# Kernel optimization log

Measured on AMD Instinct MI355X. Metric: run time of the kernel, lower is better.

The kernel has to match this reference:

```python
import jax, jax.numpy as jnp
import numpy as np

N_NODES = 200000
MAX_DEG = 128
S1, S2 = 25, 10  # neighbor sample sizes per hop (GraphSAGE defaults)


def setup_inputs() -> dict:
    key = jax.random.key(0)
    ks = jax.random.split(key, 9)
    F, H, C, B = 256, 128, 41, 1024
    return {
        "node_ids": jax.random.randint(ks[0], (B,), 0, N_NODES, dtype=jnp.int32),
        "features": jax.random.normal(ks[1], (N_NODES, F), dtype=jnp.float32),
        "adj_info": jax.random.randint(ks[2], (N_NODES, MAX_DEG), 0, N_NODES, dtype=jnp.int32),
        "W_self1": jax.random.normal(ks[3], (F, H), dtype=jnp.float32) * 0.05,
        "W_neigh1": jax.random.normal(ks[4], (F, H), dtype=jnp.float32) * 0.05,
        "W_self2": jax.random.normal(ks[5], (2 * H, H), dtype=jnp.float32) * 0.05,
        "W_neigh2": jax.random.normal(ks[6], (2 * H, H), dtype=jnp.float32) * 0.05,
        "W_pred": jax.random.normal(ks[7], (2 * H, C), dtype=jnp.float32) * 0.05,
        "b_pred": jnp.zeros((C,), dtype=jnp.float32),
    }


def _sample(adj_info, node_ids):
    """Uniform neighbor sampling: hop1 [B,S1], hop2 [B,S1,S2]."""
    k1, k2 = jax.random.split(jax.random.key(42))
    B = node_ids.shape[0]
    cols1 = jax.random.randint(k1, (B, S1), 0, MAX_DEG)
    hop1 = jnp.take_along_axis(adj_info[node_ids], cols1, axis=1)  # [B,S1]
    cols2 = jax.random.randint(k2, (B * S1, S2), 0, MAX_DEG)
    hop2 = jnp.take_along_axis(adj_info[hop1.reshape(-1)], cols2, axis=1)
    return hop1, hop2.reshape(B, S1, S2)


def _mean_agg(self_f, neigh_f, Ws, Wn, act):
    # GraphSAGE MeanAggregator with concat: [self@Ws ; mean(neigh)@Wn]
    neigh = neigh_f.mean(axis=-2)
    return act(jnp.concatenate([self_f @ Ws, neigh @ Wn], axis=-1))


def reference(node_ids, features, adj_info, W_self1, W_neigh1, W_self2, W_neigh2, W_pred, b_pred):
    hop1, hop2 = _sample(adj_info, node_ids)
    f0 = features[node_ids]      # [B,F]
    f1 = features[hop1]          # [B,S1,F]
    f2 = features[hop2]          # [B,S1,S2,F]

    h0 = _mean_agg(f0, f1, W_self1, W_neigh1, jax.nn.relu)   # [B,2H]
    h1 = _mean_agg(f1, f2, W_self1, W_neigh1, jax.nn.relu)   # [B,S1,2H]
    h = _mean_agg(h0, h1, W_self2, W_neigh2, lambda x: x)    # [B,2H]

    # tf.math.l2_normalize(x, 1): x * rsqrt(max(sum(x^2), 1e-12))
    h = h * jax.lax.rsqrt(jnp.maximum(jnp.sum(h * h, axis=1, keepdims=True), 1e-12))
    logits = h @ W_pred + b_pred
    return jax.nn.softmax(logits, axis=-1)
```

## Files before the change

### kernel.cpp

```cpp
#include <hip/hip_runtime.h>
#include <cstdint>
#include <cstddef>

#define BATCH 1024
#define S1 25
#define S2 10
#define FDIM 256
#define HDIM 128
#define NCLS 41
#define MAXDEG 128

typedef __attribute__((ext_vector_type(8))) short bf16x8;
typedef __attribute__((ext_vector_type(4))) float f32x4;

__host__ __device__ static inline void tf2x32(uint32_t k0, uint32_t k1,
                                              uint32_t c0, uint32_t c1,
                                              uint32_t& o0, uint32_t& o1) {
  const uint32_t ks2 = k0 ^ k1 ^ 0x1BD11BDAu;
  uint32_t x0 = c0 + k0, x1 = c1 + k1;
#define TFR(r) { x0 += x1; x1 = (x1 << (r)) | (x1 >> (32 - (r))); x1 ^= x0; }
  TFR(13) TFR(15) TFR(26) TFR(6)
  x0 += k1;  x1 += ks2 + 1u;
  TFR(17) TFR(29) TFR(16) TFR(24)
  x0 += ks2; x1 += k0 + 2u;
  TFR(13) TFR(15) TFR(26) TFR(6)
  x0 += k0;  x1 += k1 + 3u;
  TFR(17) TFR(29) TFR(16) TFR(24)
  x0 += k1;  x1 += ks2 + 4u;
  TFR(13) TFR(15) TFR(26) TFR(6)
  x0 += ks2; x1 += k0 + 5u;
#undef TFR
  o0 = x0; o1 = x1;
}

__device__ static inline uint32_t rand_bits_at(uint32_t kb0, uint32_t kb1, uint32_t j) {
  uint32_t o0, o1;
  tf2x32(kb0, kb1, 0u, j, o0, o1);
  return o0 ^ o1;
}

__device__ static inline ushort f2bf(float x) {
  uint32_t u = __float_as_uint(x);
  return (ushort)((u + 0x7fffu + ((u >> 16) & 1u)) >> 16);
}

__global__ __launch_bounds__(256)
void prep_kernel(const int* __restrict__ node_ids, const float* __restrict__ feat,
                 const int* __restrict__ adj,
                 const float* __restrict__ Ws1, const float* __restrict__ Wn1,
                 int* __restrict__ hop1g, ushort* __restrict__ n2m,
                 float* __restrict__ n1m, ushort* __restrict__ WbT,
                 float* __restrict__ h1m,
                 uint32_t kb1_0, uint32_t kb1_1, uint32_t kb2_0, uint32_t kb2_1) {
  const int blk = blockIdx.x;
  const int t = threadIdx.x;
  if (blk < 6400) {
    const int wave = t >> 6, lane = t & 63;
    const int g = blk * 4 + wave;
    const int b = g / S1;
    int hop1v = 0;
    if (lane == 0) {
      uint32_t c1 = rand_bits_at(kb1_0, kb1_1, (uint32_t)g) & (MAXDEG - 1);
      hop1v = adj[(size_t)node_ids[b] * MAXDEG + c1];
    }
    hop1v = __shfl(hop1v, 0, 64);
    if (lane == 0) hop1g[g] = hop1v;
    int r2id = 0;
    if (lane < S2) {
      uint32_t c2 = rand_bits_at(kb2_0, kb2_1, (uint32_t)(g * S2 + lane)) & (MAXDEG - 1);
      r2id = adj[(size_t)hop1v * MAXDEG + c2];
    }
    float4 acc = make_float4(0.f, 0.f, 0.f, 0.f);
#pragma unroll
    for (int r = 0; r < S2; ++r) {
      int rid = __shfl(r2id, r, 64);
      float4 v = ((const float4*)(feat + (size_t)rid * FDIM))[lane];
      acc.x += v.x; acc.y += v.y; acc.z += v.z; acc.w += v.w;
    }
    const float inv = 1.f / S2;
    ushort4 o;
    o.x = f2bf(acc.x * inv); o.y = f2bf(acc.y * inv);
    o.z = f2bf(acc.z * inv); o.w = f2bf(acc.w * inv);
    *(ushort4*)(n2m + (size_t)g * FDIM + lane * 4) = o;
  } else if (blk < 6656) {
    const int wave = t >> 6, lane = t & 63;
    const int b = (blk - 6400) * 4 + wave;
    int h1v = 0;
    if (lane < S1) {
      uint32_t c1 = rand_bits_at(kb1_0, kb1_1, (uint32_t)(b * S1 + lane)) & (MAXDEG - 1);
      h1v = adj[(size_t)node_ids[b] * MAXDEG + c1];
    }
    float4 acc = make_float4(0.f, 0.f, 0.f, 0.f);
#pragma unroll
    for (int r = 0; r < S1; ++r) {
      int rid = __shfl(h1v, r, 64);
      float4 v = ((const float4*)(feat + (size_t)rid * FDIM))[lane];
      acc.x += v.x; acc.y += v.y; acc.z += v.z; acc.w += v.w;
    }
    const float inv = 1.f / S1;
    acc.x *= inv; acc.y *= inv; acc.z *= inv; acc.w *= inv;
    ((float4*)(n1m + (size_t)b * FDIM))[lane] = acc;
  } else if (blk < 6912) {
    const int idx = blk - 6656;
    const int h = idx >> 7, n = idx & 127;
    const float* W = h ? Wn1 : Ws1;
    WbT[(size_t)idx * FDIM + t] = f2bf(W[(size_t)t * HDIM + n]);
  } else {
    const int i = (blk - 6912) * 256 + t;
    ((float4*)h1m)[i] = make_float4(0.f, 0.f, 0.f, 0.f);
  }
}

__global__ __launch_bounds__(256, 2)
void mfma_h1_kernel(const int* __restrict__ hop1g, const float* __restrict__ feat,
                    const ushort* __restrict__ n2m, const ushort* __restrict__ WbT,
                    float* __restrict__ h1m) {
  const int half = blockIdx.y;
  const ushort* Bmat = WbT + (size_t)half * HDIM * FDIM;
  const int m0 = blockIdx.x * 64;
  const int tid = threadIdx.x;
  const int wave = tid >> 6;
  const int lane = tid & 63;
  const int lq = lane >> 4;
  const int lr = lane & 15;

  __shared__ ushort As[64][40];
  __shared__ ushort Bs[128][40];
  __shared__ float  Cs[64][132];
  __shared__ int rowid[64];

  if (half == 0 && tid < 64) rowid[tid] = hop1g[m0 + tid];
  __syncthreads();

  f32x4 acc[4][2];
#pragma unroll
  for (int rt = 0; rt < 4; ++rt)
#pragma unroll
    for (int ct = 0; ct < 2; ++ct) acc[rt][ct] = (f32x4)(0.f);

  for (int k0 = 0; k0 < FDIM; k0 += 32) {
    const int row = tid >> 2, kc = (tid & 3) * 8;
    if (half == 0) {
      const float* rp = feat + (size_t)rowid[row] * FDIM + k0 + kc;
      float4 v0 = *(const float4*)rp;
      float4 v1 = *(const float4*)(rp + 4);
      union { ushort u[8]; int4 v; } pk;
      pk.u[0] = f2bf(v0.x); pk.u[1] = f2bf(v0.y); pk.u[2] = f2bf(v0.z); pk.u[3] = f2bf(v0.w);
      pk.u[4] = f2bf(v1.x); pk.u[5] = f2bf(v1.y); pk.u[6] = f2bf(v1.z); pk.u[7] = f2bf(v1.w);
      *(int4*)&As[row][kc] = pk.v;
    } else {
      int4 v = *(const int4*)(n2m + (size_t)(m0 + row) * FDIM + k0 + kc);
      *(int4*)&As[row][kc] = v;
    }
#pragma unroll
    for (int i = 0; i < 2; ++i) {
      int idx = tid + i * 256;
      int n = idx >> 2, kc2 = (idx & 3) * 8;
      int4 v = *(const int4*)(Bmat + (size_t)n * FDIM + k0 + kc2);
      *(int4*)&Bs[n][kc2] = v;
    }
    __syncthreads();

    bf16x8 af[4];
#pragma unroll
    for (int rt = 0; rt < 4; ++rt)
      af[rt] = *(const bf16x8*)&As[rt * 16 + lr][lq * 8];
#pragma unroll
    for (int ct = 0; ct < 2; ++ct) {
      bf16x8 bf = *(const bf16x8*)&Bs[wave * 32 + ct * 16 + lr][lq * 8];
#pragma unroll
      for (int rt = 0; rt < 4; ++rt)
        acc[rt][ct] = __builtin_amdgcn_mfma_f32_16x16x32_bf16(af[rt], bf, acc[rt][ct], 0, 0, 0);
    }
    __syncthreads();
  }

#pragma unroll
  for (int rt = 0; rt < 4; ++rt)
#pragma unroll
    for (int ct = 0; ct < 2; ++ct)
#pragma unroll
      for (int r = 0; r < 4; ++r)
        Cs[rt * 16 + lq * 4 + r][wave * 32 + ct * 16 + lr] = fmaxf(acc[rt][ct][r], 0.f);
  __syncthreads();

  if (tid < 128) {
    const int c = tid;
    const int coff = half * HDIM + c;
    float s = 0.f;
    int curb = m0 / S1;
    for (int m = 0; m < 64; ++m) {
      int b = (m0 + m) / S1;
      if (b != curb) {
        atomicAdd(&h1m[(size_t)curb * (2 * HDIM) + coff], s * (1.f / S1));
        s = 0.f; curb = b;
      }
      s += Cs[m][c];
    }
    atomicAdd(&h1m[(size_t)curb * (2 * HDIM) + coff], s * (1.f / S1));
  }
}

__global__ __launch_bounds__(256)
void tail_kernel(const int* __restrict__ node_ids, const float* __restrict__ feat,
                 const float* __restrict__ n1m, const float* __restrict__ h1m,
                 const float* __restrict__ Ws1, const float* __restrict__ Wn1,
                 const float* __restrict__ Ws2, const float* __restrict__ Wn2,
                 const float* __restrict__ Wp, const float* __restrict__ bp,
                 float* __restrict__ out) {
  const int b0 = blockIdx.x * 4;
  const int t = threadIdx.x;
  const int wave = t >> 6, lane = t & 63;

  __shared__ float A0[4][256];
  __shared__ float A1[4][256];
  __shared__ float H1[4][256];
  __shared__ float H0[4][256];
  __shared__ float HN[4][256];
  __shared__ float red[4][4];
  __shared__ float scl[4];
  __shared__ float lg[4][NCLS];
  __shared__ float sm[4][2];

  {
    const int r = wave;
    const int nid = node_ids[b0 + r];
    ((float4*)A0[r])[lane] = ((const float4*)(feat + (size_t)nid * FDIM))[lane];
    ((float4*)A1[r])[lane] = ((const float4*)(n1m + (size_t)(b0 + r) * FDIM))[lane];
    ((float4*)H1[r])[lane] = ((const float4*)(h1m + (size_t)(b0 + r) * FDIM))[lane];
  }
  __syncthreads();

  const int h = t >> 7, c = t & 127;
  {
    const float* W = h ? Wn1 : Ws1;
    const float* Ap = h ? &A1[0][0] : &A0[0][0];
    float acc[4] = {0.f, 0.f, 0.f, 0.f};
    for (int k4 = 0; k4 < 64; ++k4) {
      float w0 = W[(size_t)(k4 * 4 + 0) * HDIM + c];
      float w1 = W[(size_t)(k4 * 4 + 1) * HDIM + c];
      float w2 = W[(size_t)(k4 * 4 + 2) * HDIM + c];
      float w3 = W[(size_t)(k4 * 4 + 3) * HDIM + c];
#pragma unroll
      for (int r = 0; r < 4; ++r) {
        float4 a = ((const float4*)(Ap + r * 256))[k4];
        acc[r] += a.x * w0 + a.y * w1 + a.z * w2 + a.w * w3;
      }
    }
#pragma unroll
    for (int r = 0; r < 4; ++r) H0[r][t] = fmaxf(acc[r], 0.f);
  }
  __syncthreads();

  float hv[4];
  {
    const float* W = h ? Wn2 : Ws2;
    const float* Ap = h ? &H1[0][0] : &H0[0][0];
    float acc[4] = {0.f, 0.f, 0.f, 0.f};
    for (int k4 = 0; k4 < 64; ++k4) {
      float w0 = W[(size_t)(k4 * 4 + 0) * HDIM + c];
      float w1 = W[(size_t)(k4 * 4 + 1) * HDIM + c];
      float w2 = W[(size_t)(k4 * 4 + 2) * HDIM + c];
      float w3 = W[(size_t)(k4 * 4 + 3) * HDIM + c];
#pragma unroll
      for (int r = 0; r < 4; ++r) {
        float4 a = ((const float4*)(Ap + r * 256))[k4];
        acc[r] += a.x * w0 + a.y * w1 + a.z * w2 + a.w * w3;
      }
    }
#pragma unroll
    for (int r = 0; r < 4; ++r) hv[r] = acc[r];
  }

  {
    float ss[4];
#pragma unroll
    for (int r = 0; r < 4; ++r) ss[r] = hv[r] * hv[r];
#pragma unroll
    for (int off = 32; off; off >>= 1)
#pragma unroll
      for (int r = 0; r < 4; ++r) ss[r] += __shfl_xor(ss[r], off, 64);
    if (lane == 0) {
#pragma unroll
      for (int r = 0; r < 4; ++r) red[wave][r] = ss[r];
    }
  }
  __syncthreads();
  if (t < 4) {
    float tot = red[0][t] + red[1][t] + red[2][t] + red[3][t];
    scl[t] = rsqrtf(fmaxf(tot, 1e-12f));
  }
  __syncthreads();
#pragma unroll
  for (int r = 0; r < 4; ++r) HN[r][t] = hv[r] * scl[r];
  __syncthreads();

  int rr = 0, cc = 0;
  float logit = 0.f;
  if (t < 4 * NCLS) {
    rr = t / NCLS; cc = t - rr * NCLS;
    float acc = bp[cc];
    for (int k = 0; k < 2 * HDIM; ++k) acc += HN[rr][k] * Wp[(size_t)k * NCLS + cc];
    lg[rr][cc] = acc;
    logit = acc;
  }
  __syncthreads();
  if (t < 4) {
    float m = -1e30f;
    for (int i = 0; i < NCLS; ++i) m = fmaxf(m, lg[t][i]);
    float s = 0.f;
    for (int i = 0; i < NCLS; ++i) s += expf(lg[t][i] - m);
    sm[t][0] = m; sm[t][1] = s;
  }
  __syncthreads();
  if (t < 4 * NCLS)
    out[(size_t)(b0 + rr) * NCLS + cc] = expf(logit - sm[rr][0]) / sm[rr][1];
}

extern "C" void kernel_launch(void* const* d_in, const int* in_sizes, int n_in,
                              void* d_out, int out_size, void* d_ws, size_t ws_size,
                              hipStream_t stream) {
  const int*   node_ids = (const int*)d_in[0];
  const float* features = (const float*)d_in[1];
  const int*   adj      = (const int*)d_in[2];
  const float* Ws1      = (const float*)d_in[3];
  const float* Wn1      = (const float*)d_in[4];
  const float* Ws2      = (const float*)d_in[5];
  const float* Wn2      = (const float*)d_in[6];
  const float* Wp       = (const float*)d_in[7];
  const float* bp       = (const float*)d_in[8];
  float* out = (float*)d_out;

  char* ws = (char*)d_ws;
  int*    hop1 = (int*)(ws + 0);
  ushort* n2m  = (ushort*)(ws + 102400);
  ushort* WbT  = (ushort*)(ws + 13209600);
  float*  n1m  = (float*)(ws + 13340672);
  float*  h1m  = (float*)(ws + 14389248);

  uint32_t k1_0, k1_1, k2_0, k2_1, kb1_0, kb1_1, kb2_0, kb2_1;
  tf2x32(0u, 42u, 0u, 0u, k1_0, k1_1);
  tf2x32(0u, 42u, 0u, 1u, k2_0, k2_1);
  tf2x32(k1_0, k1_1, 0u, 1u, kb1_0, kb1_1);
  tf2x32(k2_0, k2_1, 0u, 1u, kb2_0, kb2_1);

  prep_kernel<<<7168, 256, 0, stream>>>(node_ids, features, adj, Ws1, Wn1,
                                        hop1, n2m, n1m, WbT, h1m,
                                        kb1_0, kb1_1, kb2_0, kb2_1);

  dim3 gBig(BATCH * S1 / 64, 2);
  mfma_h1_kernel<<<gBig, 256, 0, stream>>>(hop1, features, n2m, WbT, h1m);

  tail_kernel<<<BATCH / 4, 256, 0, stream>>>(node_ids, features, n1m, h1m,
                                             Ws1, Wn1, Ws2, Wn2, Wp, bp, out);
}
```

Before: 386.3 us.

## Project all node features once, then gather projected rows for aggregation

Uses the linearity of mean aggregation: instead of gathering raw hop-2 features and then multiplying, it projects the entire 200k-node feature table through Ws1/Wn1 with MFMA into a bf16 buffer. A per-batch-node aggregation kernel then does the sampling, gathers the projected rows and finishes the tail layers, which removes the atomics and intermediate buffers. The cost is a dense GEMM over every node (about 200MB of fp32 reads) in place of about 250k sampled gathers, and the hop-2 mean is taken over bf16-rounded projections.

```diff
diff --git a/kernel.cpp b/kernel.cpp
--- a/kernel.cpp
+++ b/kernel.cpp
@@ -43,80 +43,23 @@
   uint32_t u = __float_as_uint(x);
   return (ushort)((u + 0x7fffu + ((u >> 16) & 1u)) >> 16);
 }
+__device__ static inline float bf2f(ushort u) {
+  return __uint_as_float(((uint32_t)u) << 16);
+}
 
 __global__ __launch_bounds__(256)
-void prep_kernel(const int* __restrict__ node_ids, const float* __restrict__ feat,
-                 const int* __restrict__ adj,
-                 const float* __restrict__ Ws1, const float* __restrict__ Wn1,
-                 int* __restrict__ hop1g, ushort* __restrict__ n2m,
-                 float* __restrict__ n1m, ushort* __restrict__ WbT,
-                 float* __restrict__ h1m,
-                 uint32_t kb1_0, uint32_t kb1_1, uint32_t kb2_0, uint32_t kb2_1) {
-  const int blk = blockIdx.x;
-  const int t = threadIdx.x;
-  if (blk < 6400) {
-    const int wave = t >> 6, lane = t & 63;
-    const int g = blk * 4 + wave;
-    const int b = g / S1;
-    int hop1v = 0;
-    if (lane == 0) {
-      uint32_t c1 = rand_bits_at(kb1_0, kb1_1, (uint32_t)g) & (MAXDEG - 1);
-      hop1v = adj[(size_t)node_ids[b] * MAXDEG + c1];
-    }
-    hop1v = __shfl(hop1v, 0, 64);
-    if (lane == 0) hop1g[g] = hop1v;
-    int r2id = 0;
-    if (lane < S2) {
-      uint32_t c2 = rand_bits_at(kb2_0, kb2_1, (uint32_t)(g * S2 + lane)) & (MAXDEG - 1);
-      r2id = adj[(size_t)hop1v * MAXDEG + c2];
-    }
-    float4 acc = make_float4(0.f, 0.f, 0.f, 0.f);
-#pragma unroll
-    for (int r = 0; r < S2; ++r) {
-      int rid = __shfl(r2id, r, 64);
-      float4 v = ((const float4*)(feat + (size_t)rid * FDIM))[lane];
-      acc.x += v.x; acc.y += v.y; acc.z += v.z; acc.w += v.w;
-    }
-    const float inv = 1.f / S2;
-    ushort4 o;
-    o.x = f2bf(acc.x * inv); o.y = f2bf(acc.y * inv);
-    o.z = f2bf(acc.z * inv); o.w = f2bf(acc.w * inv);
-    *(ushort4*)(n2m + (size_t)g * FDIM + lane * 4) = o;
-  } else if (blk < 6656) {
-    const int wave = t >> 6, lane = t & 63;
-    const int b = (blk - 6400) * 4 + wave;
-    int h1v = 0;
-    if (lane < S1) {
-      uint32_t c1 = rand_bits_at(kb1_0, kb1_1, (uint32_t)(b * S1 + lane)) & (MAXDEG - 1);
-      h1v = adj[(size_t)node_ids[b] * MAXDEG + c1];
-    }
-    float4 acc = make_float4(0.f, 0.f, 0.f, 0.f);
-#pragma unroll
-    for (int r = 0; r < S1; ++r) {
-      int rid = __shfl(h1v, r, 64);
-      float4 v = ((const float4*)(feat + (size_t)rid * FDIM))[lane];
-      acc.x += v.x; acc.y += v.y; acc.z += v.z; acc.w += v.w;
-    }
-    const float inv = 1.f / S1;
-    acc.x *= inv; acc.y *= inv; acc.z *= inv; acc.w *= inv;
-    ((float4*)(n1m + (size_t)b * FDIM))[lane] = acc;
-  } else if (blk < 6912) {
-    const int idx = blk - 6656;
-    const int h = idx >> 7, n = idx & 127;
-    const float* W = h ? Wn1 : Ws1;
-    WbT[(size_t)idx * FDIM + t] = f2bf(W[(size_t)t * HDIM + n]);
-  } else {
-    const int i = (blk - 6912) * 256 + t;
-    ((float4*)h1m)[i] = make_float4(0.f, 0.f, 0.f, 0.f);
-  }
+void wprep_kernel(const float* __restrict__ Ws1, const float* __restrict__ Wn1,
+                  ushort* __restrict__ WbT) {
+  const int n = blockIdx.x;
+  const int k = threadIdx.x;
+  const float* W = (n < HDIM) ? Ws1 : Wn1;
+  const int c = n & (HDIM - 1);
+  WbT[(size_t)n * FDIM + k] = f2bf(W[(size_t)k * HDIM + c]);
 }
 
 __global__ __launch_bounds__(256, 2)
-void mfma_h1_kernel(const int* __restrict__ hop1g, const float* __restrict__ feat,
-                    const ushort* __restrict__ n2m, const ushort* __restrict__ WbT,
-                    float* __restrict__ h1m) {
-  const int half = blockIdx.y;
-  const ushort* Bmat = WbT + (size_t)half * HDIM * FDIM;
+void proj_kernel(const float* __restrict__ feat, const ushort* __restrict__ WbT,
+                 ushort* __restrict__ FW) {
   const int m0 = blockIdx.x * 64;
   const int tid = threadIdx.x;
   const int wave = tid >> 6;
@@ -125,39 +68,31 @@
   const int lr = lane & 15;
 
   __shared__ ushort As[64][40];
-  __shared__ ushort Bs[128][40];
+  __shared__ ushort Bs[256][40];
   __shared__ float  Cs[64][132];
-  __shared__ int rowid[64];
-
-  if (half == 0 && tid < 64) rowid[tid] = hop1g[m0 + tid];
-  __syncthreads();
-
-  f32x4 acc[4][2];
+
+  f32x4 acc[4][4];
 #pragma unroll
   for (int rt = 0; rt < 4; ++rt)
 #pragma unroll
-    for (int ct = 0; ct < 2; ++ct) acc[rt][ct] = (f32x4)(0.f);
+    for (int ct = 0; ct < 4; ++ct) acc[rt][ct] = (f32x4)(0.f);
 
   for (int k0 = 0; k0 < FDIM; k0 += 32) {
-    const int row = tid >> 2, kc = (tid & 3) * 8;
-    if (half == 0) {
-      const float* rp = feat + (size_t)rowid[row] * FDIM + k0 + kc;
+    {
+      const int row = tid >> 2, kc = (tid & 3) * 8;
+      const float* rp = feat + (size_t)(m0 + row) * FDIM + k0 + kc;
       float4 v0 = *(const float4*)rp;
       float4 v1 = *(const float4*)(rp + 4);
       union { ushort u[8]; int4 v; } pk;
       pk.u[0] = f2bf(v0.x); pk.u[1] = f2bf(v0.y); pk.u[2] = f2bf(v0.z); pk.u[3] = f2bf(v0.w);
       pk.u[4] = f2bf(v1.x); pk.u[5] = f2bf(v1.y); pk.u[6] = f2bf(v1.z); pk.u[7] = f2bf(v1.w);
       *(int4*)&As[row][kc] = pk.v;
-    } else {
-      int4 v = *(const int4*)(n2m + (size_t)(m0 + row) * FDIM + k0 + kc);
-      *(int4*)&As[row][kc] = v;
-    }
-#pragma unroll
-    for (int i = 0; i < 2; ++i) {
-      int idx = tid + i * 256;
-      int n = idx >> 2, kc2 = (idx & 3) * 8;
-      int4 v = *(const int4*)(Bmat + (size_t)n * FDIM + k0 + kc2);
-      *(int4*)&Bs[n][kc2] = v;
+    }
+#pragma unroll
+    for (int i = 0; i < 4; ++i) {
+      const int idx = tid + i * 256;
+      const int n = idx >> 2, kc = (idx & 3) * 8;
+      *(int4*)&Bs[n][kc] = *(const int4*)(WbT + (size_t)n * FDIM + k0 + kc);
     }
     __syncthreads();
 
@@ -166,8 +101,8 @@
     for (int rt = 0; rt < 4; ++rt)
       af[rt] = *(const bf16x8*)&As[rt * 16 + lr][lq * 8];
 #pragma unroll
-    for (int ct = 0; ct < 2; ++ct) {
-      bf16x8 bf = *(const bf16x8*)&Bs[wave * 32 + ct * 16 + lr][lq * 8];
+    for (int ct = 0; ct < 4; ++ct) {
+      bf16x8 bf = *(const bf16x8*)&Bs[wave * 64 + ct * 16 + lr][lq * 8];
 #pragma unroll
       for (int rt = 0; rt < 4; ++rt)
         acc[rt][ct] = __builtin_amdgcn_mfma_f32_16x16x32_bf16(af[rt], bf, acc[rt][ct], 0, 0, 0);
@@ -176,145 +111,161 @@
   }
 
 #pragma unroll
-  for (int rt = 0; rt < 4; ++rt)
-#pragma unroll
-    for (int ct = 0; ct < 2; ++ct)
-#pragma unroll
-      for (int r = 0; r < 4; ++r)
-        Cs[rt * 16 + lq * 4 + r][wave * 32 + ct * 16 + lr] = fmaxf(acc[rt][ct][r], 0.f);
-  __syncthreads();
-
-  if (tid < 128) {
-    const int c = tid;
-    const int coff = half * HDIM + c;
-    float s = 0.f;
-    int curb = m0 / S1;
-    for (int m = 0; m < 64; ++m) {
-      int b = (m0 + m) / S1;
-      if (b != curb) {
-        atomicAdd(&h1m[(size_t)curb * (2 * HDIM) + coff], s * (1.f / S1));
-        s = 0.f; curb = b;
+  for (int p = 0; p < 2; ++p) {
+    if ((wave >> 1) == p) {
+      const int cb = (wave & 1) * 64;
+#pragma unroll
+      for (int rt = 0; rt < 4; ++rt)
+#pragma unroll
+        for (int ct = 0; ct < 4; ++ct)
+#pragma unroll
+          for (int r = 0; r < 4; ++r)
+            Cs[rt * 16 + lq * 4 + r][cb + ct * 16 + lr] = acc[rt][ct][r];
+    }
+    __syncthreads();
+    {
+      const int row = tid >> 2, c0 = (tid & 3) * 32;
+      ushort* dst = FW + (size_t)(m0 + row) * FDIM + p * HDIM + c0;
+#pragma unroll
+      for (int j = 0; j < 32; j += 8) {
+        union { ushort u[8]; int4 v; } pk;
+#pragma unroll
+        for (int q = 0; q < 8; ++q) pk.u[q] = f2bf(Cs[row][c0 + j + q]);
+        *(int4*)(dst + j) = pk.v;
       }
-      s += Cs[m][c];
-    }
-    atomicAdd(&h1m[(size_t)curb * (2 * HDIM) + coff], s * (1.f / S1));
+    }
+    __syncthreads();
   }
 }
 
 __global__ __launch_bounds__(256)
-void tail_kernel(const int* __restrict__ node_ids, const float* __restrict__ feat,
-                 const float* __restrict__ n1m, const float* __restrict__ h1m,
-                 const float* __restrict__ Ws1, const float* __restrict__ Wn1,
-                 const float* __restrict__ Ws2, const float* __restrict__ Wn2,
-                 const float* __restrict__ Wp, const float* __restrict__ bp,
-                 float* __restrict__ out) {
-  const int b0 = blockIdx.x * 4;
+void agg_kernel(const int* __restrict__ node_ids, const float* __restrict__ feat,
+                const int* __restrict__ adj, const ushort* __restrict__ FW,
+                const float* __restrict__ Ws1, const float* __restrict__ Wn1,
+                const float* __restrict__ Ws2, const float* __restrict__ Wn2,
+                const float* __restrict__ Wp, const float* __restrict__ bp,
+                float* __restrict__ out,
+                uint32_t kb1_0, uint32_t kb1_1, uint32_t kb2_0, uint32_t kb2_1) {
+  const int b = blockIdx.x;
   const int t = threadIdx.x;
   const int wave = t >> 6, lane = t & 63;
 
-  __shared__ float A0[4][256];
-  __shared__ float A1[4][256];
-  __shared__ float H1[4][256];
-  __shared__ float H0[4][256];
-  __shared__ float HN[4][256];
-  __shared__ float red[4][4];
-  __shared__ float scl[4];
-  __shared__ float lg[4][NCLS];
-  __shared__ float sm[4][2];
-
+  __shared__ int   h1r[S1];
+  __shared__ int   h2r[S1 * S2];
+  __shared__ float f0s[FDIM];
+  __shared__ float redA[4][FDIM];
+  __shared__ float redB[4][FDIM];
+  __shared__ float h1m[FDIM], n1m[FDIM], h0s[FDIM], hhn[FDIM];
+  __shared__ float lgs[NCLS];
+  __shared__ float smred[4];
+  __shared__ float smax[2];
+  __shared__ int   nid_s;
+
+  if (t == 0) nid_s = node_ids[b];
+  __syncthreads();
+  const int nid = nid_s;
+  if (t < S1) {
+    uint32_t c1 = rand_bits_at(kb1_0, kb1_1, (uint32_t)(b * S1 + t)) & (MAXDEG - 1);
+    h1r[t] = adj[(size_t)nid * MAXDEG + c1];
+  }
+  if (t >= 64 && t < 128)
+    ((float4*)f0s)[t - 64] = ((const float4*)(feat + (size_t)nid * FDIM))[t - 64];
+  __syncthreads();
+  if (t < S1 * S2) {
+    uint32_t c2 = rand_bits_at(kb2_0, kb2_1, (uint32_t)(b * S1 * S2 + t)) & (MAXDEG - 1);
+    h2r[t] = adj[(size_t)h1r[t / S2] * MAXDEG + c2];
+  }
+  __syncthreads();
+
+  float sx = 0.f, sy = 0.f, nx = 0.f, ny = 0.f;
+  float4 a1 = make_float4(0.f, 0.f, 0.f, 0.f);
+  for (int l = wave; l < S1; l += 4) {
+    const int rs = h1r[l];
+    ushort2 sv = *(const ushort2*)(FW + (size_t)rs * FDIM + lane * 2);
+    float nbx = 0.f, nby = 0.f;
+    const int* hr = &h2r[l * S2];
+#pragma unroll
+    for (int s = 0; s < S2; ++s) {
+      const int rn = hr[s];
+      ushort2 nv = *(const ushort2*)(FW + (size_t)rn * FDIM + HDIM + lane * 2);
+      nbx += bf2f(nv.x); nby += bf2f(nv.y);
+    }
+    sx += fmaxf(bf2f(sv.x), 0.f);
+    sy += fmaxf(bf2f(sv.y), 0.f);
+    nx += fmaxf(nbx * (1.f / S2), 0.f);
+    ny += fmaxf(nby * (1.f / S2), 0.f);
+    float4 fv = ((const float4*)(feat + (size_t)rs * FDIM))[lane];
+    a1.x += fv.x; a1.y += fv.y; a1.z += fv.z; a1.w += fv.w;
+  }
+  redA[wave][lane * 2]            = sx;
+  redA[wave][lane * 2 + 1]        = sy;
+  redA[wave][HDIM + lane * 2]     = nx;
+  redA[wave][HDIM + lane * 2 + 1] = ny;
+  ((float4*)redB[wave])[lane] = a1;
+  __syncthreads();
   {
-    const int r = wave;
-    const int nid = node_ids[b0 + r];
-    ((float4*)A0[r])[lane] = ((const float4*)(feat + (size_t)nid * FDIM))[lane];
-    ((float4*)A1[r])[lane] = ((const float4*)(n1m + (size_t)(b0 + r) * FDIM))[lane];
-    ((float4*)H1[r])[lane] = ((const float4*)(h1m + (size_t)(b0 + r) * FDIM))[lane];
-  }
-  __syncthreads();
-
-  const int h = t >> 7, c = t & 127;
+    float v = (redA[0][t] + redA[1][t]) + (redA[2][t] + redA[3][t]);
+    h1m[t] = v * (1.f / S1);
+    float u = (redB[0][t] + redB[1][t]) + (redB[2][t] + redB[3][t]);
+    n1m[t] = u * (1.f / S1);
+  }
+  __syncthreads();
+
   {
+    const int h = t >> 7, c = t & 127;
+    const float* A = h ? n1m : f0s;
     const float* W = h ? Wn1 : Ws1;
-    const float* Ap = h ? &A1[0][0] : &A0[0][0];
-    float acc[4] = {0.f, 0.f, 0.f, 0.f};
-    for (int k4 = 0; k4 < 64; ++k4) {
-      float w0 = W[(size_t)(k4 * 4 + 0) * HDIM + c];
-      float w1 = W[(size_t)(k4 * 4 + 1) * HDIM + c];
-      float w2 = W[(size_t)(k4 * 4 + 2) * HDIM + c];
-      float w3 = W[(size_t)(k4 * 4 + 3) * HDIM + c];
-#pragma unroll
-      for (int r = 0; r < 4; ++r) {
-        float4 a = ((const float4*)(Ap + r * 256))[k4];
-        acc[r] += a.x * w0 + a.y * w1 + a.z * w2 + a.w * w3;
-      }
-    }
-#pragma unroll
-    for (int r = 0; r < 4; ++r) H0[r][t] = fmaxf(acc[r], 0.f);
-  }
-  __syncthreads();
-
-  float hv[4];
+    float acc = 0.f;
+    for (int k = 0; k < FDIM; k += 4) {
+      acc += A[k]     * W[(size_t)k       * HDIM + c]
+           + A[k + 1] * W[(size_t)(k + 1) * HDIM + c]
+           + A[k + 2] * W[(size_t)(k + 2) * HDIM + c]
+           + A[k + 3] * W[(size_t)(k + 3) * HDIM + c];
+    }
+    h0s[t] = fmaxf(acc, 0.f);
+  }
+  __syncthreads();
+
+  float hv;
   {
+    const int h = t >> 7, c = t & 127;
+    const float* A = h ? h1m : h0s;
     const float* W = h ? Wn2 : Ws2;
-    const float* Ap = h ? &H1[0][0] : &H0[0][0];
-    float acc[4] = {0.f, 0.f, 0.f, 0.f};
-    for (int k4 = 0; k4 < 64; ++k4) {
-      float w0 = W[(size_t)(k4 * 4 + 0) * HDIM + c];
-      float w1 = W[(size_t)(k4 * 4 + 1) * HDIM + c];
-      float w2 = W[(size_t)(k4 * 4 + 2) * HDIM + c];
-      float w3 = W[(size_t)(k4 * 4 + 3) * HDIM + c];
-#pragma unroll
-      for (int r = 0; r < 4; ++r) {
-        float4 a = ((const float4*)(Ap + r * 256))[k4];
-        acc[r] += a.x * w0 + a.y * w1 + a.z * w2 + a.w * w3;
-      }
-    }
-#pragma unroll
-    for (int r = 0; r < 4; ++r) hv[r] = acc[r];
-  }
-
-  {
-    float ss[4];
-#pragma unroll
-    for (int r = 0; r < 4; ++r) ss[r] = hv[r] * hv[r];
-#pragma unroll
-    for (int off = 32; off; off >>= 1)
-#pragma unroll
-      for (int r = 0; r < 4; ++r) ss[r] += __shfl_xor(ss[r], off, 64);
-    if (lane == 0) {
-#pragma unroll
-      for (int r = 0; r < 4; ++r) red[wave][r] = ss[r];
-    }
-  }
-  __syncthreads();
-  if (t < 4) {
-    float tot = red[0][t] + red[1][t] + red[2][t] + red[3][t];
-    scl[t] = rsqrtf(fmaxf(tot, 1e-12f));
-  }
-  __syncthreads();
-#pragma unroll
-  for (int r = 0; r < 4; ++r) HN[r][t] = hv[r] * scl[r];
-  __syncthreads();
-
-  int rr = 0, cc = 0;
-  float logit = 0.f;
-  if (t < 4 * NCLS) {
-    rr = t / NCLS; cc = t - rr * NCLS;
-    float acc = bp[cc];
-    for (int k = 0; k < 2 * HDIM; ++k) acc += HN[rr][k] * Wp[(size_t)k * NCLS + cc];
-    lg[rr][cc] = acc;
-    logit = acc;
-  }
-  __syncthreads();
-  if (t < 4) {
+    float acc = 0.f;
+    for (int k = 0; k < FDIM; k += 4) {
+      acc += A[k]     * W[(size_t)k       * HDIM + c]
+           + A[k + 1] * W[(size_t)(k + 1) * HDIM + c]
+           + A[k + 2] * W[(size_t)(k + 2) * HDIM + c]
+           + A[k + 3] * W[(size_t)(k + 3) * HDIM + c];
+    }
+    hv = acc;
+  }
+  float ss = hv * hv;
+#pragma unroll
+  for (int off = 32; off; off >>= 1) ss += __shfl_xor(ss, off, 64);
+  if (lane == 0) smred[wave] = ss;
+  __syncthreads();
+  if (t == 0)
+    smax[0] = rsqrtf(fmaxf(smred[0] + smred[1] + smred[2] + smred[3], 1e-12f));
+  __syncthreads();
+  hhn[t] = hv * smax[0];
+  __syncthreads();
+
+  if (t < NCLS) {
+    float acc = bp[t];
+    for (int k = 0; k < 2 * HDIM; ++k) acc += hhn[k] * Wp[(size_t)k * NCLS + t];
+    lgs[t] = acc;
+  }
+  __syncthreads();
+  if (t == 0) {
     float m = -1e30f;
-    for (int i = 0; i < NCLS; ++i) m = fmaxf(m, lg[t][i]);
+    for (int i = 0; i < NCLS; ++i) m = fmaxf(m, lgs[i]);
     float s = 0.f;
-    for (int i = 0; i < NCLS; ++i) s += expf(lg[t][i] - m);
-    sm[t][0] = m; sm[t][1] = s;
-  }
-  __syncthreads();
-  if (t < 4 * NCLS)
-    out[(size_t)(b0 + rr) * NCLS + cc] = expf(logit - sm[rr][0]) / sm[rr][1];
+    for (int i = 0; i < NCLS; ++i) s += expf(lgs[i] - m);
+    smax[0] = m; smax[1] = s;
+  }
+  __syncthreads();
+  if (t < NCLS) out[(size_t)b * NCLS + t] = expf(lgs[t] - smax[0]) / smax[1];
 }
 
 extern "C" void kernel_launch(void* const* d_in, const int* in_sizes, int n_in,
@@ -332,11 +283,8 @@
   float* out = (float*)d_out;
 
   char* ws = (char*)d_ws;
-  int*    hop1 = (int*)(ws + 0);
-  ushort* n2m  = (ushort*)(ws + 102400);
-  ushort* WbT  = (ushort*)(ws + 13209600);
-  float*  n1m  = (float*)(ws + 13340672);
-  float*  h1m  = (float*)(ws + 14389248);
+  ushort* WbT = (ushort*)(ws + 0);
+  ushort* FW  = (ushort*)(ws + 131072);
 
   uint32_t k1_0, k1_1, k2_0, k2_1, kb1_0, kb1_1, kb2_0, kb2_1;
   tf2x32(0u, 42u, 0u, 0u, k1_0, k1_1);
@@ -344,13 +292,9 @@
   tf2x32(k1_0, k1_1, 0u, 1u, kb1_0, kb1_1);
   tf2x32(k2_0, k2_1, 0u, 1u, kb2_0, kb2_1);
 
-  prep_kernel<<<7168, 256, 0, stream>>>(node_ids, features, adj, Ws1, Wn1,
-                                        hop1, n2m, n1m, WbT, h1m,
+  wprep_kernel<<<256, 256, 0, stream>>>(Ws1, Wn1, WbT);
+  proj_kernel<<<200000 / 64, 256, 0, stream>>>(features, WbT, FW);
+  agg_kernel<<<BATCH, 256, 0, stream>>>(node_ids, features, adj, FW,
+                                        Ws1, Wn1, Ws2, Wn2, Wp, bp, out,
                                         kb1_0, kb1_1, kb2_0, kb2_1);
-
-  dim3 gBig(BATCH * S1 / 64, 2);
-  mfma_h1_kernel<<<gBig, 256, 0, stream>>>(hop1, features, n2m, WbT, h1m);
-
-  tail_kernel<<<BATCH / 4, 256, 0, stream>>>(node_ids, features, n1m, h1m,
-                                             Ws1, Wn1, Ws2, Wn2, Wp, bp, out);
-}
+}
```

After: 434.6 us. 12.5% more time.
